# Performance work log

Measured on AMD Instinct MI355X. Metric: run time of the kernel, lower is better.

Reference implementation:

```python
import jax, jax.numpy as jnp
import numpy as np

N_NODES = 50000
N_EDGES = 800000
D = 128
N_LAYERS = 4
N_GRAPHS = 512
N_CLASS = 10


def setup_inputs() -> dict:
    key = jax.random.key(0)
    ks = jax.random.split(key, 12)
    x = jax.random.normal(ks[0], (N_NODES, D), dtype=jnp.float32)
    edge_index = jax.random.randint(ks[1], (2, N_EDGES), 0, N_NODES, dtype=jnp.int64)
    batch = jnp.sort(jax.random.randint(ks[2], (N_NODES,), 0, N_GRAPHS, dtype=jnp.int64))
    s = 1.0 / np.sqrt(D)
    W_conv = jax.random.uniform(ks[3], (N_LAYERS, D, D), jnp.float32, -s, s)
    b_conv = jnp.zeros((N_LAYERS, D), jnp.float32)
    W1 = jax.random.uniform(ks[4], (D, D), jnp.float32, -s, s)
    b1 = jnp.zeros((D,), jnp.float32)
    W2 = jax.random.uniform(ks[5], (D, D // 2), jnp.float32, -s, s)
    b2 = jnp.zeros((D // 2,), jnp.float32)
    W3 = jax.random.uniform(ks[6], (D // 2, N_CLASS), jnp.float32, -1.0 / np.sqrt(D // 2), 1.0 / np.sqrt(D // 2))
    b3 = jnp.zeros((N_CLASS,), jnp.float32)
    return {"x": x, "edge_index": edge_index, "batch": batch,
            "W_conv": W_conv, "b_conv": b_conv,
            "W1": W1, "b1": b1, "W2": W2, "b2": b2, "W3": W3, "b3": b3}


def reference(x, edge_index, batch, W_conv, b_conv, W1, b1, W2, b2, W3, b3):
    row, col = edge_index[0], edge_index[1]  # messages: source=row -> target=col
    # GCN symmetric normalization with self-loops (PyG GCNConv default).
    deg = jax.ops.segment_sum(jnp.ones((row.shape[0],), x.dtype), col, num_segments=N_NODES) + 1.0
    dinv = jax.lax.rsqrt(deg)
    edge_norm = (dinv[row] * dinv[col])[:, None]      # [E,1]
    self_norm = (1.0 / deg)[:, None]                  # [N,1] = dinv_i * dinv_i

    def gcn_layer(h, W, b):
        h = h @ W                                      # [N,D]
        agg = jax.ops.segment_sum(h[row] * edge_norm, col, num_segments=N_NODES)
        agg = agg + h * self_norm                      # self-loop contribution
        return jax.nn.relu(agg + b)

    h = x
    for l in range(N_LAYERS):
        h = gcn_layer(h, W_conv[l], b_conv[l])

    # global_add_pool over graph ids
    g = jax.ops.segment_sum(h, batch, num_segments=N_GRAPHS)  # [G,D]

    # MLP head (dropout is identity in eval mode)
    g = jax.nn.relu(g @ W1 + b1)
    g = jax.nn.relu(g @ W2 + b2)
    return g @ W3 + b3
```

## Files before the change

kernel.cpp:

```cpp
#include <hip/hip_runtime.h>
#include <stdint.h>
#include <stddef.h>

#define NN 50000
#define NE 800000
#define DD 128
#define NL 4
#define NG 512
#define NC 10
#define NB 196
#define BCAP 5056

using short8 = __attribute__((ext_vector_type(8))) short;
using f32x4  = __attribute__((ext_vector_type(4))) float;

__device__ __forceinline__ float bf2f(unsigned short u) {
  union { unsigned int i; float f; } c; c.i = ((unsigned int)u) << 16; return c.f;
}
__device__ __forceinline__ unsigned short f2bf(float f) {
  union { unsigned int i; float f; } c; c.f = f;
  unsigned int i = c.i;
  return (unsigned short)((i + 0x7FFFu + ((i >> 16) & 1u)) >> 16);
}
__device__ __forceinline__ unsigned int pack2(float a, float b) {
  return (unsigned int)f2bf(a) | ((unsigned int)f2bf(b) << 16);
}

__global__ __launch_bounds__(1024) void p1a_k(const int* __restrict__ ecol,
                                              int* __restrict__ hist) {
  __shared__ int lh[NB];
  int tid = threadIdx.x;
  if (tid < NB) lh[tid] = 0;
  __syncthreads();
  int e0 = blockIdx.x * 4096 + tid;
#pragma unroll
  for (int j = 0; j < 4; ++j) {
    int e = e0 + j * 1024;
    if (e < NE) atomicAdd(&lh[ecol[e] >> 8], 1);
  }
  __syncthreads();
  if (tid < NB && lh[tid] > 0) atomicAdd(&hist[tid], lh[tid]);
}

__global__ __launch_bounds__(256) void scanb_k(const int* __restrict__ hist,
                                               int* __restrict__ ebase,
                                               int* __restrict__ cursor,
                                               int* __restrict__ csr_ptr) {
  __shared__ int sc[256];
  int t = threadIdx.x;
  int h = (t < NB) ? hist[t] : 0;
  sc[t] = h; __syncthreads();
  for (int off = 1; off < 256; off <<= 1) {
    int v = (t >= off) ? sc[t - off] : 0;
    __syncthreads();
    sc[t] += v;
    __syncthreads();
  }
  if (t < NB) { ebase[t] = sc[t] - h; cursor[t] = sc[t] - h; }
  if (t == NB - 1) ebase[NB] = sc[t];
  if (t == 0) csr_ptr[NN] = NE;
}

__global__ __launch_bounds__(1024) void p1b_k(const int* __restrict__ erow,
                                              const int* __restrict__ ecol,
                                              int* __restrict__ cursor,
                                              unsigned int* __restrict__ ebuf) {
  __shared__ int lcnt[NB], gb[NB];
  int tid = threadIdx.x;
  if (tid < NB) lcnt[tid] = 0;
  __syncthreads();
  int e0 = blockIdx.x * 4096 + tid;
  int bk[4], sl[4]; unsigned int pk[4];
#pragma unroll
  for (int j = 0; j < 4; ++j) {
    int e = e0 + j * 1024;
    bk[j] = -1;
    if (e < NE) {
      int d = ecol[e], s = erow[e];
      bk[j] = d >> 8;
      pk[j] = ((unsigned int)(d & 255) << 16) | (unsigned int)s;
      sl[j] = atomicAdd(&lcnt[bk[j]], 1);
    }
  }
  __syncthreads();
  if (tid < NB) {
    int c = lcnt[tid];
    gb[tid] = c ? atomicAdd(&cursor[tid], c) : 0;
  }
  __syncthreads();
#pragma unroll
  for (int j = 0; j < 4; ++j)
    if (bk[j] >= 0) ebuf[gb[bk[j]] + sl[j]] = pk[j];
}

__global__ __launch_bounds__(1024) void p2_k(const unsigned int* __restrict__ ebuf,
                                             const int* __restrict__ ebase,
                                             const float* __restrict__ x,
                                             int* __restrict__ csr_ptr,
                                             int* __restrict__ csr_src,
                                             float* __restrict__ dinv,
                                             unsigned short* __restrict__ xb) {
  __shared__ unsigned int pr[BCAP];
  __shared__ int srcb[BCAP];
  __shared__ int hist_s[256], scn[256], lcur[256];
  __shared__ float dinv_s[256];
  int b = blockIdx.x, tid = threadIdx.x;
  int beg = ebase[b];
  int cnt = ebase[b + 1] - beg;
  if (cnt > BCAP) cnt = BCAP;

  if (tid < 256) hist_s[tid] = 0;
  __syncthreads();
  for (int i = tid; i < cnt; i += 1024) {
    unsigned int p = ebuf[beg + i];
    pr[i] = p;
    atomicAdd(&hist_s[p >> 16], 1);
  }
  __syncthreads();
  if (tid < 256) scn[tid] = hist_s[tid];
  __syncthreads();
  for (int off = 1; off < 256; off <<= 1) {
    int v = (tid < 256 && tid >= off) ? scn[tid - off] : 0;
    __syncthreads();
    if (tid < 256) scn[tid] += v;
    __syncthreads();
  }
  if (tid < 256) {
    int ex = scn[tid] - hist_s[tid];
    lcur[tid] = ex;
    int V = b * 256 + tid;
    if (V < NN) {
      csr_ptr[V] = beg + ex;
      float dv = rsqrtf((float)(hist_s[tid] + 1));
      dinv[V] = dv;
      dinv_s[tid] = dv;
    }
  }
  __syncthreads();
  for (int i = tid; i < cnt; i += 1024) {
    unsigned int p = pr[i];
    int pos = atomicAdd(&lcur[p >> 16], 1);
    srcb[pos] = (int)(p & 0xFFFFu);
  }
  __syncthreads();
  for (int i = tid; i < cnt; i += 1024) csr_src[beg + i] = srcb[i];

  for (int i4 = tid; i4 < 256 * 32; i4 += 1024) {
    int vl = i4 >> 5;
    int V = b * 256 + vl;
    if (V < NN) {
      float d = dinv_s[vl];
      f32x4 vx = *((const f32x4*)(x + (size_t)V * DD) + (i4 & 31));
      uint2 o;
      o.x = pack2(vx[0] * d, vx[1] * d);
      o.y = pack2(vx[2] * d, vx[3] * d);
      *((uint2*)(xb + (size_t)V * DD) + (i4 & 31)) = o;
    }
  }
}

__global__ void gptr_k(const int* __restrict__ batch, int* __restrict__ gptr) {
  int i = blockIdx.x * 256 + threadIdx.x;
  if (i >= NN) return;
  int b  = batch[i];
  int bp = (i == 0) ? -1 : batch[i - 1];
  for (int g = bp + 1; g <= b; ++g) gptr[g] = i;
  if (i == NN - 1) { for (int g = b + 1; g <= NG; ++g) gptr[g] = NN; }
}

__global__ __launch_bounds__(256) void agg_k(const unsigned short* __restrict__ hs,
                                             unsigned short* __restrict__ agg,
                                             const int* __restrict__ csr_ptr,
                                             const int* __restrict__ csr_src,
                                             const float* __restrict__ dinv) {
  int v = blockIdx.x * 4 + (threadIdx.x >> 6);
  if (v >= NN) return;
  int lane = threadIdx.x & 63;
  int qg = lane >> 4, r = lane & 15;
  const uint4* rows = (const uint4*)hs;

  float a0 = 0.f, a1 = 0.f, a2 = 0.f, a3 = 0.f, a4 = 0.f, a5 = 0.f, a6 = 0.f, a7 = 0.f;
  float b0 = 0.f, b1 = 0.f, b2 = 0.f, b3 = 0.f, b4 = 0.f, b5 = 0.f, b6 = 0.f, b7 = 0.f;
  if (qg == 0) {
    uint4 p = rows[(size_t)v * 16 + r];
    a0 = bf2f((unsigned short)(p.x & 0xffffu)); a1 = bf2f((unsigned short)(p.x >> 16));
    a2 = bf2f((unsigned short)(p.y & 0xffffu)); a3 = bf2f((unsigned short)(p.y >> 16));
    a4 = bf2f((unsigned short)(p.z & 0xffffu)); a5 = bf2f((unsigned short)(p.z >> 16));
    a6 = bf2f((unsigned short)(p.w & 0xffffu)); a7 = bf2f((unsigned short)(p.w >> 16));
  }

  int e = csr_ptr[v] + qg, end = csr_ptr[v + 1];
  for (; e + 4 < end; e += 8) {
    int s0 = csr_src[e];
    int s1 = csr_src[e + 4];
    uint4 p = rows[(size_t)s0 * 16 + r];
    uint4 q = rows[(size_t)s1 * 16 + r];
    a0 += bf2f((unsigned short)(p.x & 0xffffu)); a1 += bf2f((unsigned short)(p.x >> 16));
    a2 += bf2f((unsigned short)(p.y & 0xffffu)); a3 += bf2f((unsigned short)(p.y >> 16));
    a4 += bf2f((unsigned short)(p.z & 0xffffu)); a5 += bf2f((unsigned short)(p.z >> 16));
    a6 += bf2f((unsigned short)(p.w & 0xffffu)); a7 += bf2f((unsigned short)(p.w >> 16));
    b0 += bf2f((unsigned short)(q.x & 0xffffu)); b1 += bf2f((unsigned short)(q.x >> 16));
    b2 += bf2f((unsigned short)(q.y & 0xffffu)); b3 += bf2f((unsigned short)(q.y >> 16));
    b4 += bf2f((unsigned short)(q.z & 0xffffu)); b5 += bf2f((unsigned short)(q.z >> 16));
    b6 += bf2f((unsigned short)(q.w & 0xffffu)); b7 += bf2f((unsigned short)(q.w >> 16));
  }
  if (e < end) {
    int s0 = csr_src[e];
    uint4 p = rows[(size_t)s0 * 16 + r];
    a0 += bf2f((unsigned short)(p.x & 0xffffu)); a1 += bf2f((unsigned short)(p.x >> 16));
    a2 += bf2f((unsigned short)(p.y & 0xffffu)); a3 += bf2f((unsigned short)(p.y >> 16));
    a4 += bf2f((unsigned short)(p.z & 0xffffu)); a5 += bf2f((unsigned short)(p.z >> 16));
    a6 += bf2f((unsigned short)(p.w & 0xffffu)); a7 += bf2f((unsigned short)(p.w >> 16));
  }
  a0 += b0; a1 += b1; a2 += b2; a3 += b3; a4 += b4; a5 += b5; a6 += b6; a7 += b7;

  a0 += __shfl_xor(a0, 16, 64); a0 += __shfl_xor(a0, 32, 64);
  a1 += __shfl_xor(a1, 16, 64); a1 += __shfl_xor(a1, 32, 64);
  a2 += __shfl_xor(a2, 16, 64); a2 += __shfl_xor(a2, 32, 64);
  a3 += __shfl_xor(a3, 16, 64); a3 += __shfl_xor(a3, 32, 64);
  a4 += __shfl_xor(a4, 16, 64); a4 += __shfl_xor(a4, 32, 64);
  a5 += __shfl_xor(a5, 16, 64); a5 += __shfl_xor(a5, 32, 64);
  a6 += __shfl_xor(a6, 16, 64); a6 += __shfl_xor(a6, 32, 64);
  a7 += __shfl_xor(a7, 16, 64); a7 += __shfl_xor(a7, 32, 64);

  if (qg == 0) {
    float dv = dinv[v];
    uint4 o;
    o.x = pack2(dv * a0, dv * a1);
    o.y = pack2(dv * a2, dv * a3);
    o.z = pack2(dv * a4, dv * a5);
    o.w = pack2(dv * a6, dv * a7);
    *((uint4*)(agg + (size_t)v * DD) + r) = o;
  }
}

__global__ __launch_bounds__(256) void gemm_relu_k(const unsigned short* __restrict__ A,
                                                   const float* __restrict__ W,
                                                   const float* __restrict__ bias,
                                                   unsigned short* __restrict__ out,
                                                   const float* __restrict__ dscale,
                                                   int M) {
  __shared__ unsigned short Wt[128][136];
  int tid = threadIdx.x;
  for (int i = tid; i < 128 * 128; i += 256) {
    int k = i >> 7, n = i & 127;
    Wt[n][k] = f2bf(W[i]);
  }
  __syncthreads();

  int wave = tid >> 6, lane = tid & 63;
  int q = lane >> 4, r = lane & 15;
  int row0 = blockIdx.x * 64 + wave * 16;

  int arow = row0 + r;
  if (arow > M - 1) arow = M - 1;
  const short* Arow = (const short*)A + (size_t)arow * DD;

  short8 afrag[4];
#pragma unroll
  for (int ks = 0; ks < 4; ++ks)
    afrag[ks] = *(const short8*)(Arow + ks * 32 + q * 8);

  f32x4 acc[8];
#pragma unroll
  for (int ct = 0; ct < 8; ++ct) acc[ct] = (f32x4){0.f, 0.f, 0.f, 0.f};

#pragma unroll
  for (int ks = 0; ks < 4; ++ks) {
#pragma unroll
    for (int ct = 0; ct < 8; ++ct) {
      short8 bfrag = *(const short8*)(&Wt[ct * 16 + r][ks * 32 + q * 8]);
      acc[ct] = __builtin_amdgcn_mfma_f32_16x16x32_bf16(afrag[ks], bfrag, acc[ct], 0, 0, 0);
    }
  }

  int orow = row0 + q * 4;
  float sc[4];
#pragma unroll
  for (int reg = 0; reg < 4; ++reg) {
    int rr = orow + reg;
    sc[reg] = (dscale && rr < M) ? dscale[rr] : 1.f;
  }
#pragma unroll
  for (int ct = 0; ct < 8; ++ct) {
    int coln = ct * 16 + r;
    float bc = bias[coln];
#pragma unroll
    for (int reg = 0; reg < 4; ++reg) {
      int rr = orow + reg;
      if (rr < M) {
        float val = fmaxf(acc[ct][reg] + bc, 0.f) * sc[reg];
        out[(size_t)rr * DD + coln] = f2bf(val);
      }
    }
  }
}

__global__ __launch_bounds__(128) void pool_k(const unsigned short* __restrict__ h,
                                              const int* __restrict__ gptr,
                                              float* __restrict__ gpool) {
  int g = blockIdx.x, t = threadIdx.x;
  int beg = gptr[g], end = gptr[g + 1];
  float acc = 0.f;
  for (int v = beg; v < end; ++v) acc += bf2f(h[(size_t)v * DD + t]);
  gpool[g * DD + t] = acc;
}

__global__ __launch_bounds__(128) void mlp_k(const float* __restrict__ gpool,
                                             const float* __restrict__ W1,
                                             const float* __restrict__ b1,
                                             const float* __restrict__ W2,
                                             const float* __restrict__ b2,
                                             const float* __restrict__ W3,
                                             const float* __restrict__ b3,
                                             float* __restrict__ out) {
  __shared__ float s_g[128], s_h1[128], s_h2[64];
  int g = blockIdx.x, t = threadIdx.x;
  s_g[t] = gpool[g * DD + t];
  __syncthreads();
  {
    float a = b1[t];
    for (int k = 0; k < 128; ++k) a += s_g[k] * W1[k * 128 + t];
    s_h1[t] = fmaxf(a, 0.f);
  }
  __syncthreads();
  if (t < 64) {
    float a = b2[t];
    for (int k = 0; k < 128; ++k) a += s_h1[k] * W2[k * 64 + t];
    s_h2[t] = fmaxf(a, 0.f);
  }
  __syncthreads();
  if (t < NC) {
    float a = b3[t];
    for (int k = 0; k < 64; ++k) a += s_h2[k] * W3[k * NC + t];
    out[g * NC + t] = a;
  }
}


extern "C" void kernel_launch(void* const* d_in, const int* in_sizes, int n_in,
                              void* d_out, int out_size, void* d_ws, size_t ws_size,
                              hipStream_t stream) {
  const float* x     = (const float*)d_in[0];
  const int*   ei    = (const int*)d_in[1];
  const int*   batch = (const int*)d_in[2];
  const float* Wc    = (const float*)d_in[3];
  const float* bc    = (const float*)d_in[4];
  const float* W1    = (const float*)d_in[5];
  const float* b1    = (const float*)d_in[6];
  const float* W2    = (const float*)d_in[7];
  const float* b2    = (const float*)d_in[8];
  const float* W3    = (const float*)d_in[9];
  const float* b3    = (const float*)d_in[10];
  float* out = (float*)d_out;

  const int* erow = ei;
  const int* ecol = ei + NE;

  char* w = (char*)d_ws;
  int*   hist    = (int*)w;    w += NB * 4;
  int*   cursor  = (int*)w;    w += NB * 4;
  int*   ebase   = (int*)w;    w += (NB + 4) * 4;
  int*   csr_ptr = (int*)w;    w += (size_t)(NN + 4) * 4;
  int*   gptr    = (int*)w;    w += (NG + 4) * 4;
  int*   csr_src = (int*)w;    w += (size_t)NE * 4;
  float* dinv    = (float*)w;  w += (size_t)NN * 4;
  float* gpool   = (float*)w;  w += (size_t)NG * DD * 4;
  w = (char*)(((uintptr_t)w + 255) & ~(uintptr_t)255);
  unsigned short* xb   = (unsigned short*)w; w += (size_t)NN * DD * 2;
  unsigned short* aggb = (unsigned short*)w; w += (size_t)NN * DD * 2;
  unsigned short* hbuf = (unsigned short*)w; w += (size_t)NN * DD * 2;
  unsigned int* ebuf = (unsigned int*)aggb;

  hipMemsetAsync(d_ws, 0, NB * 2 * 4, stream);

  p1a_k  <<<NB, 1024, 0, stream>>>(ecol, hist);
  scanb_k<<<1, 256, 0, stream>>>(hist, ebase, cursor, csr_ptr);
  p1b_k  <<<NB, 1024, 0, stream>>>(erow, ecol, cursor, ebuf);
  p2_k   <<<NB, 1024, 0, stream>>>(ebuf, ebase, x, csr_ptr, csr_src, dinv, xb);
  gptr_k <<<(NN + 255) / 256, 256, 0, stream>>>(batch, gptr);

  const int aggGrid  = (NN + 3) / 4;
  const int gemmGrid = (NN + 63) / 64;

  for (int l = 0; l < NL; ++l) {
    const unsigned short* hin = (l == 0) ? xb : hbuf;
    const float* dsc = (l == NL - 1) ? nullptr : dinv;
    agg_k<<<aggGrid, 256, 0, stream>>>(hin, aggb, csr_ptr, csr_src, dinv);
    gemm_relu_k<<<gemmGrid, 256, 0, stream>>>(aggb, Wc + (size_t)l * DD * DD,
                                              bc + (size_t)l * DD, hbuf, dsc, NN);
  }

  pool_k<<<NG, 128, 0, stream>>>(hbuf, gptr, gpool);
  mlp_k <<<NG, 128, 0, stream>>>(gpool, W1, b1, W2, b2, W3, b3, out);

  (void)in_sizes; (void)n_in; (void)out_size; (void)ws_size;
}
```

Baseline: 366.6 us.

## Fuse neighbor aggregation and GEMM into one per-layer kernel via shared memory

Merges the separate aggregation and bf16 MFMA GEMM kernels into a single layer kernel. Each 64-row block gathers and sums neighbor rows into a shared-memory tile, then multiplies that tile by the weight matrix. Output ping-pongs between two buffers. This removes the round trip of the aggregated activations through global memory and one launch per layer. The cost is a different gather mapping: each node is now handled by 16 threads with a serial edge loop instead of a full wave, which may lower memory-level parallelism and worsen load imbalance inside a block.

Result: slower. 442.3 us (+20.6%).

```diff
diff --git a/kernel.cpp b/kernel.cpp
--- a/kernel.cpp
+++ b/kernel.cpp
@@ -24,6 +24,12 @@
 }
 __device__ __forceinline__ unsigned int pack2(float a, float b) {
   return (unsigned int)f2bf(a) | ((unsigned int)f2bf(b) << 16);
+}
+__device__ __forceinline__ void acc8(float* a, uint4 p) {
+  a[0] += bf2f((unsigned short)(p.x & 0xffffu)); a[1] += bf2f((unsigned short)(p.x >> 16));
+  a[2] += bf2f((unsigned short)(p.y & 0xffffu)); a[3] += bf2f((unsigned short)(p.y >> 16));
+  a[4] += bf2f((unsigned short)(p.z & 0xffffu)); a[5] += bf2f((unsigned short)(p.z >> 16));
+  a[6] += bf2f((unsigned short)(p.w & 0xffffu)); a[7] += bf2f((unsigned short)(p.w >> 16));
 }
 
 __global__ __launch_bounds__(1024) void p1a_k(const int* __restrict__ ecol,
@@ -168,98 +174,63 @@
   if (i == NN - 1) { for (int g = b + 1; g <= NG; ++g) gptr[g] = NN; }
 }
 
-__global__ __launch_bounds__(256) void agg_k(const unsigned short* __restrict__ hs,
-                                             unsigned short* __restrict__ agg,
-                                             const int* __restrict__ csr_ptr,
-                                             const int* __restrict__ csr_src,
-                                             const float* __restrict__ dinv) {
-  int v = blockIdx.x * 4 + (threadIdx.x >> 6);
-  if (v >= NN) return;
-  int lane = threadIdx.x & 63;
-  int qg = lane >> 4, r = lane & 15;
-  const uint4* rows = (const uint4*)hs;
-
-  float a0 = 0.f, a1 = 0.f, a2 = 0.f, a3 = 0.f, a4 = 0.f, a5 = 0.f, a6 = 0.f, a7 = 0.f;
-  float b0 = 0.f, b1 = 0.f, b2 = 0.f, b3 = 0.f, b4 = 0.f, b5 = 0.f, b6 = 0.f, b7 = 0.f;
-  if (qg == 0) {
-    uint4 p = rows[(size_t)v * 16 + r];
-    a0 = bf2f((unsigned short)(p.x & 0xffffu)); a1 = bf2f((unsigned short)(p.x >> 16));
-    a2 = bf2f((unsigned short)(p.y & 0xffffu)); a3 = bf2f((unsigned short)(p.y >> 16));
-    a4 = bf2f((unsigned short)(p.z & 0xffffu)); a5 = bf2f((unsigned short)(p.z >> 16));
-    a6 = bf2f((unsigned short)(p.w & 0xffffu)); a7 = bf2f((unsigned short)(p.w >> 16));
-  }
-
-  int e = csr_ptr[v] + qg, end = csr_ptr[v + 1];
-  for (; e + 4 < end; e += 8) {
-    int s0 = csr_src[e];
-    int s1 = csr_src[e + 4];
-    uint4 p = rows[(size_t)s0 * 16 + r];
-    uint4 q = rows[(size_t)s1 * 16 + r];
-    a0 += bf2f((unsigned short)(p.x & 0xffffu)); a1 += bf2f((unsigned short)(p.x >> 16));
-    a2 += bf2f((unsigned short)(p.y & 0xffffu)); a3 += bf2f((unsigned short)(p.y >> 16));
-    a4 += bf2f((unsigned short)(p.z & 0xffffu)); a5 += bf2f((unsigned short)(p.z >> 16));
-    a6 += bf2f((unsigned short)(p.w & 0xffffu)); a7 += bf2f((unsigned short)(p.w >> 16));
-    b0 += bf2f((unsigned short)(q.x & 0xffffu)); b1 += bf2f((unsigned short)(q.x >> 16));
-    b2 += bf2f((unsigned short)(q.y & 0xffffu)); b3 += bf2f((unsigned short)(q.y >> 16));
-    b4 += bf2f((unsigned short)(q.z & 0xffffu)); b5 += bf2f((unsigned short)(q.z >> 16));
-    b6 += bf2f((unsigned short)(q.w & 0xffffu)); b7 += bf2f((unsigned short)(q.w >> 16));
-  }
-  if (e < end) {
-    int s0 = csr_src[e];
-    uint4 p = rows[(size_t)s0 * 16 + r];
-    a0 += bf2f((unsigned short)(p.x & 0xffffu)); a1 += bf2f((unsigned short)(p.x >> 16));
-    a2 += bf2f((unsigned short)(p.y & 0xffffu)); a3 += bf2f((unsigned short)(p.y >> 16));
-    a4 += bf2f((unsigned short)(p.z & 0xffffu)); a5 += bf2f((unsigned short)(p.z >> 16));
-    a6 += bf2f((unsigned short)(p.w & 0xffffu)); a7 += bf2f((unsigned short)(p.w >> 16));
-  }
-  a0 += b0; a1 += b1; a2 += b2; a3 += b3; a4 += b4; a5 += b5; a6 += b6; a7 += b7;
-
-  a0 += __shfl_xor(a0, 16, 64); a0 += __shfl_xor(a0, 32, 64);
-  a1 += __shfl_xor(a1, 16, 64); a1 += __shfl_xor(a1, 32, 64);
-  a2 += __shfl_xor(a2, 16, 64); a2 += __shfl_xor(a2, 32, 64);
-  a3 += __shfl_xor(a3, 16, 64); a3 += __shfl_xor(a3, 32, 64);
-  a4 += __shfl_xor(a4, 16, 64); a4 += __shfl_xor(a4, 32, 64);
-  a5 += __shfl_xor(a5, 16, 64); a5 += __shfl_xor(a5, 32, 64);
-  a6 += __shfl_xor(a6, 16, 64); a6 += __shfl_xor(a6, 32, 64);
-  a7 += __shfl_xor(a7, 16, 64); a7 += __shfl_xor(a7, 32, 64);
-
-  if (qg == 0) {
-    float dv = dinv[v];
-    uint4 o;
-    o.x = pack2(dv * a0, dv * a1);
-    o.y = pack2(dv * a2, dv * a3);
-    o.z = pack2(dv * a4, dv * a5);
-    o.w = pack2(dv * a6, dv * a7);
-    *((uint4*)(agg + (size_t)v * DD) + r) = o;
-  }
-}
-
-__global__ __launch_bounds__(256) void gemm_relu_k(const unsigned short* __restrict__ A,
-                                                   const float* __restrict__ W,
-                                                   const float* __restrict__ bias,
-                                                   unsigned short* __restrict__ out,
-                                                   const float* __restrict__ dscale,
-                                                   int M) {
+__global__ __launch_bounds__(256) void layer_k(const unsigned short* __restrict__ hs,
+                                               const float* __restrict__ W,
+                                               const float* __restrict__ bias,
+                                               unsigned short* __restrict__ out,
+                                               const int* __restrict__ csr_ptr,
+                                               const int* __restrict__ csr_src,
+                                               const float* __restrict__ dinv,
+                                               int last) {
   __shared__ unsigned short Wt[128][136];
+  __shared__ unsigned short aggS[64][136];
   int tid = threadIdx.x;
+
   for (int i = tid; i < 128 * 128; i += 256) {
     int k = i >> 7, n = i & 127;
     Wt[n][k] = f2bf(W[i]);
   }
+
+  int row0 = blockIdx.x * 64;
+  int qi = tid >> 4, r = tid & 15;
+  const uint4* rows = (const uint4*)hs;
+
+#pragma unroll
+  for (int j = 0; j < 4; ++j) {
+    int nb = qi * 4 + j;
+    int v = row0 + nb;
+    float a[8] = {0.f, 0.f, 0.f, 0.f, 0.f, 0.f, 0.f, 0.f};
+    if (v < NN) {
+      acc8(a, rows[(size_t)v * 16 + r]);
+      int e = csr_ptr[v], end = csr_ptr[v + 1];
+      for (; e + 3 < end; e += 4) {
+        int s0 = csr_src[e], s1 = csr_src[e + 1], s2 = csr_src[e + 2], s3 = csr_src[e + 3];
+        uint4 p0 = rows[(size_t)s0 * 16 + r];
+        uint4 p1 = rows[(size_t)s1 * 16 + r];
+        uint4 p2 = rows[(size_t)s2 * 16 + r];
+        uint4 p3 = rows[(size_t)s3 * 16 + r];
+        acc8(a, p0); acc8(a, p1); acc8(a, p2); acc8(a, p3);
+      }
+      for (; e < end; ++e) acc8(a, rows[(size_t)csr_src[e] * 16 + r]);
+      float dv = dinv[v];
+#pragma unroll
+      for (int t = 0; t < 8; ++t) a[t] *= dv;
+    }
+    uint4 o;
+    o.x = pack2(a[0], a[1]); o.y = pack2(a[2], a[3]);
+    o.z = pack2(a[4], a[5]); o.w = pack2(a[6], a[7]);
+    *(uint4*)&aggS[nb][r * 8] = o;
+  }
   __syncthreads();
 
   int wave = tid >> 6, lane = tid & 63;
-  int q = lane >> 4, r = lane & 15;
-  int row0 = blockIdx.x * 64 + wave * 16;
-
-  int arow = row0 + r;
-  if (arow > M - 1) arow = M - 1;
-  const short* Arow = (const short*)A + (size_t)arow * DD;
+  int q = lane >> 4, rr16 = lane & 15;
+  int wrow0 = row0 + wave * 16;
 
   short8 afrag[4];
 #pragma unroll
   for (int ks = 0; ks < 4; ++ks)
-    afrag[ks] = *(const short8*)(Arow + ks * 32 + q * 8);
+    afrag[ks] = *(const short8*)(&aggS[wave * 16 + rr16][ks * 32 + q * 8]);
 
   f32x4 acc[8];
 #pragma unroll
@@ -269,26 +240,26 @@
   for (int ks = 0; ks < 4; ++ks) {
 #pragma unroll
     for (int ct = 0; ct < 8; ++ct) {
-      short8 bfrag = *(const short8*)(&Wt[ct * 16 + r][ks * 32 + q * 8]);
+      short8 bfrag = *(const short8*)(&Wt[ct * 16 + rr16][ks * 32 + q * 8]);
       acc[ct] = __builtin_amdgcn_mfma_f32_16x16x32_bf16(afrag[ks], bfrag, acc[ct], 0, 0, 0);
     }
   }
 
-  int orow = row0 + q * 4;
+  int orow = wrow0 + q * 4;
   float sc[4];
 #pragma unroll
   for (int reg = 0; reg < 4; ++reg) {
     int rr = orow + reg;
-    sc[reg] = (dscale && rr < M) ? dscale[rr] : 1.f;
+    sc[reg] = (!last && rr < NN) ? dinv[rr] : 1.f;
   }
 #pragma unroll
   for (int ct = 0; ct < 8; ++ct) {
-    int coln = ct * 16 + r;
+    int coln = ct * 16 + rr16;
     float bc = bias[coln];
 #pragma unroll
     for (int reg = 0; reg < 4; ++reg) {
       int rr = orow + reg;
-      if (rr < M) {
+      if (rr < NN) {
         float val = fmaxf(acc[ct][reg] + bc, 0.f) * sc[reg];
         out[(size_t)rr * DD + coln] = f2bf(val);
       }
@@ -367,10 +338,10 @@
   float* dinv    = (float*)w;  w += (size_t)NN * 4;
   float* gpool   = (float*)w;  w += (size_t)NG * DD * 4;
   w = (char*)(((uintptr_t)w + 255) & ~(uintptr_t)255);
-  unsigned short* xb   = (unsigned short*)w; w += (size_t)NN * DD * 2;
-  unsigned short* aggb = (unsigned short*)w; w += (size_t)NN * DD * 2;
-  unsigned short* hbuf = (unsigned short*)w; w += (size_t)NN * DD * 2;
-  unsigned int* ebuf = (unsigned int*)aggb;
+  unsigned short* xb = (unsigned short*)w; w += (size_t)NN * DD * 2;
+  unsigned short* hA = (unsigned short*)w; w += (size_t)NN * DD * 2;
+  unsigned short* hB = (unsigned short*)w; w += (size_t)NN * DD * 2;
+  unsigned int* ebuf = (unsigned int*)hA;
 
   hipMemsetAsync(d_ws, 0, NB * 2 * 4, stream);
 
@@ -380,18 +351,17 @@
   p2_k   <<<NB, 1024, 0, stream>>>(ebuf, ebase, x, csr_ptr, csr_src, dinv, xb);
   gptr_k <<<(NN + 255) / 256, 256, 0, stream>>>(batch, gptr);
 
-  const int aggGrid  = (NN + 3) / 4;
-  const int gemmGrid = (NN + 63) / 64;
-
+  const int layerGrid = (NN + 63) / 64;
+
+  const unsigned short* src[NL] = {xb, hA, hB, hA};
+  unsigned short*       dst[NL] = {hA, hB, hA, hB};
   for (int l = 0; l < NL; ++l) {
-    const unsigned short* hin = (l == 0) ? xb : hbuf;
-    const float* dsc = (l == NL - 1) ? nullptr : dinv;
-    agg_k<<<aggGrid, 256, 0, stream>>>(hin, aggb, csr_ptr, csr_src, dinv);
-    gemm_relu_k<<<gemmGrid, 256, 0, stream>>>(aggb, Wc + (size_t)l * DD * DD,
-                                              bc + (size_t)l * DD, hbuf, dsc, NN);
-  }
-
-  pool_k<<<NG, 128, 0, stream>>>(hbuf, gptr, gpool);
+    layer_k<<<layerGrid, 256, 0, stream>>>(src[l], Wc + (size_t)l * DD * DD,
+                                           bc + (size_t)l * DD, dst[l],
+                                           csr_ptr, csr_src, dinv, (l == NL - 1) ? 1 : 0);
+  }
+
+  pool_k<<<NG, 128, 0, stream>>>(dst[NL - 1], gptr, gpool);
   mlp_k <<<NG, 128, 0, stream>>>(gpool, W1, b1, W2, b2, W3, b3, out);
 
   (void)in_sizes; (void)n_in; (void)out_size; (void)ws_size;
```
